# Kernel optimization log

Measured on AMD Instinct MI355X. Metric: run time of the kernel, lower is better.

The kernel has to match this reference:

```python
import jax, jax.numpy as jnp
import numpy as np

NUM_CLASSES = 1000
N, C = 8192, 256

def setup_inputs() -> dict:
    key = jax.random.key(0)
    k1, k2, k3 = jax.random.split(key, 3)
    p = jax.random.normal(k1, (N, C), dtype=jnp.float32)
    z = jax.random.normal(k2, (N, C), dtype=jnp.float32)
    t = jax.random.uniform(k3, (N, NUM_CLASSES), dtype=jnp.float32, minval=1e-4, maxval=1.0)
    targets = t / jnp.sum(t, axis=1, keepdims=True)  # valid soft-label distribution
    return {"p": p, "z": z, "targets": targets}

def reference(p, z, targets):
    z = jax.lax.stop_gradient(z)  # z.detach()
    # F.normalize(dim=1), eps=1e-12
    p = p / jnp.maximum(jnp.linalg.norm(p, axis=1, keepdims=True), 1e-12)
    zn = z / jnp.maximum(jnp.linalg.norm(z, axis=1, keepdims=True), 1e-12)
    dot_product = -jnp.matmul(p, zn.T)  # [N, N]
    # entropy of soft targets, NaN rows (any exact-zero entry) zeroed
    prod = targets * jnp.log(targets)
    entr = -jnp.sum(prod, axis=1)
    entr = jnp.where(jnp.isnan(entr), 0.0, entr)
    norm_entr = entr / jnp.log(jnp.float32(NUM_CLASSES))
    r = 1.0 - norm_entr
    mask1 = jnp.outer(r, r)  # [N, N]
    # cosine similarity Gram of targets (torch cosine_similarity eps=1e-8)
    tnorm = jnp.linalg.norm(targets, axis=1)
    denom = jnp.maximum(tnorm[:, None] * tnorm[None, :], 1e-8)
    mask2 = jnp.matmul(targets, targets.T) / denom  # [N, N]
    n = dot_product.shape[0]
    mask_anchor_out = 1.0 - jnp.eye(n, dtype=dot_product.dtype)
    mask_combined = mask1 * mask2 * mask_anchor_out
    sel = dot_product * mask_combined
    # mean over nonzero entries (jit-safe: sum / count of nonzeros)
    nz = (sel != 0.0)
    return jnp.sum(sel) / jnp.sum(nz).astype(sel.dtype)
```

## Files before the change

kernel.cpp:

```cpp
#include <hip/hip_runtime.h>
#include <math.h>

#define NROWS 8192
#define CDIM 256
#define KDIM 1000
#define KPAD 1024

#define BC 128
#define BK 64
#define BI 8

typedef __attribute__((ext_vector_type(8))) short bf16x8;
typedef __attribute__((ext_vector_type(4))) float f32x4;
typedef _Float16 f16;
typedef __attribute__((ext_vector_type(4))) _Float16 f16x4;

__device__ __forceinline__ unsigned short f2bf(float x) {
  unsigned int u = __float_as_uint(x);
  u += 0x7fffu + ((u >> 16) & 1u);
  return (unsigned short)(u >> 16);
}
__device__ __forceinline__ float bf2f(unsigned short h) {
  return __uint_as_float(((unsigned int)h) << 16);
}

__device__ __forceinline__ void gl16(const void* g, void* l) {
  __builtin_amdgcn_global_load_lds(
      (const __attribute__((address_space(1))) unsigned int*)g,
      (__attribute__((address_space(3))) unsigned int*)l, 16, 0, 0);
}

__global__ __launch_bounds__(256, 4) void prep_kernel(
    const float* __restrict__ p, const float* __restrict__ z,
    const float* __restrict__ t,
    unsigned short* __restrict__ gAhi, unsigned short* __restrict__ gAlo,
    unsigned short* __restrict__ gBhi, unsigned short* __restrict__ gBlo,
    unsigned short* __restrict__ gUhi, unsigned short* __restrict__ gUlo,
    float* __restrict__ diag) {
  __shared__ float tbuf[8 * 1028];
  __shared__ float st_s[8], uu_s[8], sa_s[8], sb_s[8];
  __shared__ double r_s[8];
  const int tid = threadIdx.x;
  const int w = tid >> 6, lane = tid & 63;
  const int stripe = blockIdx.x;
  const int istep = stripe >> 2;
  const int qtr = stripe & 3;
  const int i0 = stripe * 8;

#pragma unroll
  for (int rr = 0; rr < 2; ++rr) {
    const int row = 2 * w + rr;
    const float* trow = t + (size_t)(i0 + row) * KDIM;
    float stt = 0.f, ent = 0.f, zfl = 0.f;
#pragma unroll
    for (int c = 0; c < 4; ++c) {
      const int k4 = c * 64 + lane;
      float4 v = make_float4(0.f, 0.f, 0.f, 0.f);
      if (k4 < 250) {
        v = *(const float4*)(trow + k4 * 4);
        const float vv[4] = {v.x, v.y, v.z, v.w};
#pragma unroll
        for (int q = 0; q < 4; ++q) {
          stt += vv[q] * vv[q];
          if (vv[q] > 0.f) ent += vv[q] * logf(vv[q]);
          else zfl = 1.f;
        }
      }
      *(float4*)&tbuf[row * 1028 + k4 * 4] = v;
    }
#pragma unroll
    for (int off = 32; off; off >>= 1) {
      stt += __shfl_xor(stt, off);
      ent += __shfl_xor(ent, off);
      zfl += __shfl_xor(zfl, off);
    }
    if (lane == 0) {
      const float tnorm = sqrtf(stt);
      st_s[row] = 1.f / tnorm;
      uu_s[row] = stt / (tnorm * tnorm);
      const float entr = (zfl > 0.f) ? 0.f : (-ent);
      r_s[row] = 1.0 - (double)entr / log(1000.0);
    }
  }
  __syncthreads();

#pragma unroll
  for (int it = 0; it < 4; ++it) {
    const int item = it * 256 + tid;
    const int kt = item >> 7;
    const int kf = (item >> 4) & 7;
    const int cl = item & 15;
    const int kcl = kf * 16 + cl;
    unsigned int hi[4], lo[4];
#pragma unroll
    for (int q = 0; q < 4; ++q) {
      const int r0 = 2 * q, r1 = r0 + 1;
      const float v0 = tbuf[r0 * 1028 + kt * 128 + kcl] * st_s[r0];
      const float v1 = tbuf[r1 * 1028 + kt * 128 + kcl] * st_s[r1];
      const unsigned short h0 = f2bf(v0), h1 = f2bf(v1);
      hi[q] = (unsigned int)h0 | ((unsigned int)h1 << 16);
      const unsigned short e0 = f2bf(v0 - bf2f(h0));
      const unsigned short e1 = f2bf(v1 - bf2f(h1));
      lo[q] = (unsigned int)e0 | ((unsigned int)e1 << 16);
    }
    const size_t off = ((size_t)(kt * 256 + istep)) * 8192
                       + (size_t)kf * 1024 + (size_t)(qtr * 16 + cl) * 16;
    *(uint4*)((char*)gUhi + off) = make_uint4(hi[0], hi[1], hi[2], hi[3]);
    *(uint4*)((char*)gUlo + off) = make_uint4(lo[0], lo[1], lo[2], lo[3]);
  }
  __syncthreads();

  float* ptile = tbuf;
  float* ztile = tbuf + 8 * 260;
#pragma unroll
  for (int rr = 0; rr < 2; ++rr) {
    const int row = 2 * w + rr;
    const float* prow = p + (size_t)(i0 + row) * CDIM;
    const float* zrow = z + (size_t)(i0 + row) * CDIM;
    const float4 pv = *(const float4*)(prow + lane * 4);
    const float4 zv = *(const float4*)(zrow + lane * 4);
    *(float4*)&ptile[row * 260 + lane * 4] = pv;
    *(float4*)&ztile[row * 260 + lane * 4] = zv;
    float sp = pv.x * pv.x + pv.y * pv.y + pv.z * pv.z + pv.w * pv.w;
    float sz = zv.x * zv.x + zv.y * zv.y + zv.z * zv.z + zv.w * zv.w;
    float spz = pv.x * zv.x + pv.y * zv.y + pv.z * zv.z + pv.w * zv.w;
#pragma unroll
    for (int off = 32; off; off >>= 1) {
      sp += __shfl_xor(sp, off);
      sz += __shfl_xor(sz, off);
      spz += __shfl_xor(spz, off);
    }
    if (lane == 0) {
      const double r = r_s[row];
      const float pnorm = sqrtf(sp), znorm = sqrtf(sz);
      const float sav = (float)(r / fmax((double)pnorm, 1e-12));
      const float sbv = (float)(r / fmax((double)znorm, 1e-12));
      sa_s[row] = sav; sb_s[row] = sbv;
      diag[i0 + row] = spz * sav * sbv * uu_s[row];
    }
  }
  __syncthreads();

  {
    const int cfg = tid >> 4;
    const int cl = tid & 15;
    const int crd = cfg * 16 + cl;
#pragma unroll 1
    for (int which = 0; which < 2; ++which) {
      const float* tile = which ? ztile : ptile;
      const float* ss = which ? sb_s : sa_s;
      unsigned short* ghi = which ? gBhi : gAhi;
      unsigned short* glo = which ? gBlo : gAlo;
      unsigned int hi[4], lo[4];
#pragma unroll
      for (int q = 0; q < 4; ++q) {
        const int r0 = 2 * q, r1 = r0 + 1;
        const float v0 = tile[r0 * 260 + crd] * ss[r0];
        const float v1 = tile[r1 * 260 + crd] * ss[r1];
        const unsigned short h0 = f2bf(v0), h1 = f2bf(v1);
        hi[q] = (unsigned int)h0 | ((unsigned int)h1 << 16);
        const unsigned short e0 = f2bf(v0 - bf2f(h0));
        const unsigned short e1 = f2bf(v1 - bf2f(h1));
        lo[q] = (unsigned int)e0 | ((unsigned int)e1 << 16);
      }
      const size_t off = ((size_t)((cfg >> 3) * 256 + istep)) * 8192
                         + (size_t)(cfg & 7) * 1024 + (size_t)(qtr * 16 + cl) * 16;
      *(uint4*)((char*)ghi + off) = make_uint4(hi[0], hi[1], hi[2], hi[3]);
      *(uint4*)((char*)glo + off) = make_uint4(lo[0], lo[1], lo[2], lo[3]);
    }
  }
}

__global__ __launch_bounds__(256, 1) void mfma_gemm_kernel(
    const unsigned short* __restrict__ gAhi, const unsigned short* __restrict__ gAlo,
    const unsigned short* __restrict__ gBhi, const unsigned short* __restrict__ gBlo,
    const unsigned short* __restrict__ gUhi, const unsigned short* __restrict__ gUlo,
    f16* __restrict__ part1, f16* __restrict__ part2, int steps) {
  __shared__ unsigned short lds[3][6][4096];
  const int tid = threadIdx.x;
  const int lane = tid & 63;
  const int wid = tid >> 6;
  const int wr = wid >> 1, wc = wid & 1;
  const int ct = blockIdx.x, kt = blockIdx.y, zc = blockIdx.z;
  const int istep0 = zc * steps;

  f32x4 acc1[4][4], acc2[4][4];
#pragma unroll
  for (int c = 0; c < 4; ++c)
#pragma unroll
    for (int k = 0; k < 4; ++k) {
      acc1[c][k] = (f32x4){0.f, 0.f, 0.f, 0.f};
      acc2[c][k] = (f32x4){0.f, 0.f, 0.f, 0.f};
    }

  const char* sP[6] = {(const char*)gAhi, (const char*)gAlo,
                       (const char*)gBhi, (const char*)gBlo,
                       (const char*)gUhi, (const char*)gUlo};

  auto stage = [&](int buf, int s) {
    const size_t ab = ((size_t)(ct * 256 + istep0 + s)) * 8192 + (size_t)tid * 16;
    const size_t ub = ((size_t)(kt * 256 + istep0 + s)) * 8192 + (size_t)tid * 16;
#pragma unroll
    for (int pl = 0; pl < 4; ++pl) {
      gl16(sP[pl] + ab, &lds[buf][pl][tid * 8]);
      gl16(sP[pl] + ab + 4096, &lds[buf][pl][(tid + 256) * 8]);
    }
#pragma unroll
    for (int pl = 4; pl < 6; ++pl) {
      gl16(sP[pl] + ub, &lds[buf][pl][tid * 8]);
      gl16(sP[pl] + ub + 4096, &lds[buf][pl][(tid + 256) * 8]);
    }
  };

  stage(0, 0);
  if (steps > 1) stage(1, 1);
  for (int s = 0; s < steps; ++s) {
    const int cur = s % 3;
    if (s < steps - 1) {
      asm volatile("s_waitcnt vmcnt(12)" ::: "memory");
    } else {
      asm volatile("s_waitcnt vmcnt(0)" ::: "memory");
    }
    __builtin_amdgcn_s_barrier();
    asm volatile("" ::: "memory");
    if (s + 2 < steps) stage((s + 2) % 3, s + 2);

    bf16x8 ah[4], al[4], bh[4], bl[4];
#pragma unroll
    for (int c = 0; c < 4; ++c) {
      const int cf = wr * 4 + c;
      ah[c] = *(const bf16x8*)&lds[cur][0][(cf * 64 + lane) * 8];
      al[c] = *(const bf16x8*)&lds[cur][1][(cf * 64 + lane) * 8];
      bh[c] = *(const bf16x8*)&lds[cur][2][(cf * 64 + lane) * 8];
      bl[c] = *(const bf16x8*)&lds[cur][3][(cf * 64 + lane) * 8];
    }
    __builtin_amdgcn_s_setprio(1);
#pragma unroll
    for (int kh = 0; kh < 2; ++kh) {
      bf16x8 uh[2], ul[2];
#pragma unroll
      for (int k2 = 0; k2 < 2; ++k2) {
        const int kf = wc * 4 + kh * 2 + k2;
        uh[k2] = *(const bf16x8*)&lds[cur][4][(kf * 64 + lane) * 8];
        ul[k2] = *(const bf16x8*)&lds[cur][5][(kf * 64 + lane) * 8];
      }
#pragma unroll
      for (int k2 = 0; k2 < 2; ++k2) {
        const int k = kh * 2 + k2;
#pragma unroll
        for (int c = 0; c < 4; ++c) {
          acc1[c][k] = __builtin_amdgcn_mfma_f32_16x16x32_bf16(ah[c], uh[k2], acc1[c][k], 0, 0, 0);
          acc1[c][k] = __builtin_amdgcn_mfma_f32_16x16x32_bf16(al[c], uh[k2], acc1[c][k], 0, 0, 0);
          acc1[c][k] = __builtin_amdgcn_mfma_f32_16x16x32_bf16(ah[c], ul[k2], acc1[c][k], 0, 0, 0);
          acc2[c][k] = __builtin_amdgcn_mfma_f32_16x16x32_bf16(bh[c], uh[k2], acc2[c][k], 0, 0, 0);
          acc2[c][k] = __builtin_amdgcn_mfma_f32_16x16x32_bf16(bl[c], uh[k2], acc2[c][k], 0, 0, 0);
          acc2[c][k] = __builtin_amdgcn_mfma_f32_16x16x32_bf16(bh[c], ul[k2], acc2[c][k], 0, 0, 0);
        }
      }
    }
    __builtin_amdgcn_s_setprio(0);
  }

  f16* o1 = part1 + (size_t)zc * (CDIM * KPAD);
  f16* o2 = part2 + (size_t)zc * (CDIM * KPAD);
#pragma unroll
  for (int c = 0; c < 4; ++c)
#pragma unroll
    for (int k = 0; k < 4; ++k)
#pragma unroll
      for (int j = 0; j < 4; ++j) {
        const int cg = ct * 128 + (wr * 4 + c) * 16 + (lane >> 4) * 4 + j;
        const int kg = kt * 128 + (wc * 4 + k) * 16 + (lane & 15);
        o1[(size_t)cg * KPAD + kg] = (f16)acc1[c][k][j];
        o2[(size_t)cg * KPAD + kg] = (f16)acc2[c][k][j];
      }
}

__global__ __launch_bounds__(256) void reduce_h_kernel(
    const f16* __restrict__ part1, const f16* __restrict__ part2,
    double* __restrict__ bsum, int split) {
  const int tid = threadIdx.x;
  const size_t base = ((size_t)blockIdx.x * 256 + tid) * 4;
  double m1[4] = {0, 0, 0, 0}, m2[4] = {0, 0, 0, 0};
#pragma unroll 4
  for (int zz = 0; zz < split; ++zz) {
    const f16x4 a = *(const f16x4*)(part1 + (size_t)zz * (CDIM * KPAD) + base);
    const f16x4 b = *(const f16x4*)(part2 + (size_t)zz * (CDIM * KPAD) + base);
#pragma unroll
    for (int e = 0; e < 4; ++e) {
      m1[e] += (double)(float)a[e];
      m2[e] += (double)(float)b[e];
    }
  }
  double s = 0.0;
#pragma unroll
  for (int e = 0; e < 4; ++e) s += m1[e] * m2[e];
  __shared__ double red[256];
  red[tid] = s;
  __syncthreads();
  for (int off = 128; off; off >>= 1) {
    if (tid < off) red[tid] += red[tid + off];
    __syncthreads();
  }
  if (tid == 0) bsum[blockIdx.x] = red[0];
}

__global__ __launch_bounds__(256) void rowstats_kernel(
    const float* __restrict__ p, const float* __restrict__ z,
    const float* __restrict__ t,
    float* __restrict__ sa, float* __restrict__ sb,
    float* __restrict__ st, float* __restrict__ diag) {
  const int i = blockIdx.x;
  const int tid = threadIdx.x;
  const float pv = p[(size_t)i * CDIM + tid];
  const float zv = z[(size_t)i * CDIM + tid];
  float sp = pv * pv, sz = zv * zv, spz = pv * zv;
  float stt = 0.f, ent = 0.f, zfl = 0.f;
  const float* trow = t + (size_t)i * KDIM;
  for (int k = tid; k < KDIM; k += 256) {
    const float tv = trow[k];
    stt += tv * tv;
    if (tv > 0.f) ent += tv * logf(tv);
    else zfl = 1.f;
  }
#pragma unroll
  for (int off = 32; off; off >>= 1) {
    sp  += __shfl_down(sp, off);
    sz  += __shfl_down(sz, off);
    spz += __shfl_down(spz, off);
    stt += __shfl_down(stt, off);
    ent += __shfl_down(ent, off);
    zfl += __shfl_down(zfl, off);
  }
  __shared__ float wred[4][6];
  const int wid = tid >> 6, lane = tid & 63;
  if (lane == 0) {
    wred[wid][0] = sp;  wred[wid][1] = sz;  wred[wid][2] = spz;
    wred[wid][3] = stt; wred[wid][4] = ent; wred[wid][5] = zfl;
  }
  __syncthreads();
  if (tid == 0) {
    sp  = wred[0][0] + wred[1][0] + wred[2][0] + wred[3][0];
    sz  = wred[0][1] + wred[1][1] + wred[2][1] + wred[3][1];
    spz = wred[0][2] + wred[1][2] + wred[2][2] + wred[3][2];
    stt = wred[0][3] + wred[1][3] + wred[2][3] + wred[3][3];
    ent = wred[0][4] + wred[1][4] + wred[2][4] + wred[3][4];
    zfl = wred[0][5] + wred[1][5] + wred[2][5] + wred[3][5];
    const float pnorm = sqrtf(sp);
    const float znorm = sqrtf(sz);
    const float tnorm = sqrtf(stt);
    const float entr = (zfl > 0.f) ? 0.f : (-ent);
    const double r = 1.0 - (double)entr / log(1000.0);
    const float sav = (float)(r / fmax((double)pnorm, 1e-12));
    const float sbv = (float)(r / fmax((double)znorm, 1e-12));
    const float stv = 1.f / tnorm;
    const float uu = stt / (tnorm * tnorm);
    sa[i] = sav; sb[i] = sbv; st[i] = stv;
    diag[i] = spz * sav * sbv * uu;
  }
}

__global__ __launch_bounds__(256) void fp32_gemm_kernel(
    const float* __restrict__ p, const float* __restrict__ z,
    const float* __restrict__ t,
    const float* __restrict__ sa, const float* __restrict__ sb,
    const float* __restrict__ st,
    float* __restrict__ part1, float* __restrict__ part2, int ichunk) {
  __shared__ float As[BI][BC];
  __shared__ float Bs[BI][BC];
  __shared__ float Us[BI][BK];
  const int tid = threadIdx.x;
  const int c0 = blockIdx.x * BC;
  const int k0 = blockIdx.y * BK;
  const int i0 = blockIdx.z * ichunk;
  float acc1[8][4] = {{0.f}};
  float acc2[8][4] = {{0.f}};
  const int tc = tid & 15;
  const int tk = tid >> 4;
  const int lrow = tid >> 5;
  const int lcolA = (tid & 31) * 4;
  const int lcolU = (tid & 31) * 2;
  for (int ib = 0; ib < ichunk; ib += BI) {
    const int i = i0 + ib + lrow;
    const float sav = sa[i], sbv = sb[i], stv = st[i];
    const float4 pv = *(const float4*)(p + (size_t)i * CDIM + c0 + lcolA);
    const float4 zv = *(const float4*)(z + (size_t)i * CDIM + c0 + lcolA);
    const int kk = k0 + lcolU;
    const float u0 = (kk     < KDIM) ? t[(size_t)i * KDIM + kk]     * stv : 0.f;
    const float u1 = (kk + 1 < KDIM) ? t[(size_t)i * KDIM + kk + 1] * stv : 0.f;
    __syncthreads();
    *(float4*)&As[lrow][lcolA] = make_float4(pv.x * sav, pv.y * sav, pv.z * sav, pv.w * sav);
    *(float4*)&Bs[lrow][lcolA] = make_float4(zv.x * sbv, zv.y * sbv, zv.z * sbv, zv.w * sbv);
    Us[lrow][lcolU] = u0;
    Us[lrow][lcolU + 1] = u1;
    __syncthreads();
#pragma unroll
    for (int ii = 0; ii < BI; ++ii) {
      const float4 a0 = *(const float4*)&As[ii][tc * 8];
      const float4 a1 = *(const float4*)&As[ii][tc * 8 + 4];
      const float4 b0 = *(const float4*)&Bs[ii][tc * 8];
      const float4 b1 = *(const float4*)&Bs[ii][tc * 8 + 4];
      const float4 u  = *(const float4*)&Us[ii][tk * 4];
      const float a[8] = {a0.x, a0.y, a0.z, a0.w, a1.x, a1.y, a1.z, a1.w};
      const float b[8] = {b0.x, b0.y, b0.z, b0.w, b1.x, b1.y, b1.z, b1.w};
      const float uv[4] = {u.x, u.y, u.z, u.w};
#pragma unroll
      for (int m = 0; m < 8; ++m)
#pragma unroll
        for (int n = 0; n < 4; ++n) {
          acc1[m][n] = fmaf(a[m], uv[n], acc1[m][n]);
          acc2[m][n] = fmaf(b[m], uv[n], acc2[m][n]);
        }
    }
  }
  float* o1 = part1 + (size_t)blockIdx.z * (CDIM * KPAD);
  float* o2 = part2 + (size_t)blockIdx.z * (CDIM * KPAD);
#pragma unroll
  for (int m = 0; m < 8; ++m) {
    const int c = c0 + tc * 8 + m;
    const int k = k0 + tk * 4;
    *(float4*)&o1[(size_t)c * KPAD + k] = *(const float4*)acc1[m];
    *(float4*)&o2[(size_t)c * KPAD + k] = *(const float4*)acc2[m];
  }
}

__global__ __launch_bounds__(256) void reduce_kernel(
    const float* __restrict__ part1, const float* __restrict__ part2,
    double* __restrict__ bsum, int split) {
  const int tid = threadIdx.x;
  double s = 0.0;
  for (int r = 0; r < 4; ++r) {
    const size_t idx = (size_t)blockIdx.x * 1024 + (size_t)r * 256 + tid;
    double m1 = 0.0, m2 = 0.0;
    for (int zz = 0; zz < split; ++zz) {
      m1 += (double)part1[(size_t)zz * (CDIM * KPAD) + idx];
      m2 += (double)part2[(size_t)zz * (CDIM * KPAD) + idx];
    }
    s += m1 * m2;
  }
  __shared__ double red[256];
  red[tid] = s;
  __syncthreads();
  for (int off = 128; off; off >>= 1) {
    if (tid < off) red[tid] += red[tid + off];
    __syncthreads();
  }
  if (tid == 0) bsum[blockIdx.x] = red[0];
}

__global__ __launch_bounds__(256) void final_kernel(
    const double* __restrict__ bsum, const float* __restrict__ diag,
    float* __restrict__ out, int nb) {
  const int tid = threadIdx.x;
  double s = 0.0;
  for (int i = tid; i < nb; i += 256) s += bsum[i];
  double d = 0.0;
  for (int i = tid; i < NROWS; i += 256) d += (double)diag[i];
  __shared__ double red[256];
  red[tid] = s;
  __syncthreads();
  for (int off = 128; off; off >>= 1) {
    if (tid < off) red[tid] += red[tid + off];
    __syncthreads();
  }
  double s_all = red[0];
  __syncthreads();
  red[tid] = d;
  __syncthreads();
  for (int off = 128; off; off >>= 1) {
    if (tid < off) red[tid] += red[tid + off];
    __syncthreads();
  }
  if (tid == 0) {
    const double s_diag = red[0];
    const double sel_sum = -(s_all - s_diag);
    const double cnt = (double)NROWS * (double)NROWS - (double)NROWS;
    out[0] = (float)(sel_sum / cnt);
  }
}

extern "C" void kernel_launch(void* const* d_in, const int* in_sizes, int n_in,
                              void* d_out, int out_size, void* d_ws, size_t ws_size,
                              hipStream_t stream) {
  const float* p = (const float*)d_in[0];
  const float* z = (const float*)d_in[1];
  const float* t = (const float*)d_in[2];
  float* out = (float*)d_out;
  char* ws = (char*)d_ws;

  float* sa = (float*)ws;
  float* sb = sa + NROWS;
  float* st = sb + NROWS;
  float* diag = st + NROWS;
  const size_t statsB = (size_t)4 * NROWS * sizeof(float);

  const size_t planeA = (size_t)2 * 256 * 8 * 1024;
  const size_t planeU = (size_t)8 * 256 * 8 * 1024;
  const size_t chunkH = (size_t)CDIM * KPAD * 2;
  const size_t chunkF = (size_t)CDIM * KPAD * 4;

  int split = 16;
  while (split > 4 &&
         statsB + 4 * planeA + 2 * planeU + (size_t)split * 2 * chunkH + 8192 > ws_size)
    split >>= 1;
  const bool use_mfma =
      statsB + 4 * planeA + 2 * planeU + (size_t)split * 2 * chunkH + 8192 <= ws_size;

  if (use_mfma) {
    char* base = ws + statsB;
    unsigned short* gAhi = (unsigned short*)(base);
    unsigned short* gAlo = (unsigned short*)(base + planeA);
    unsigned short* gBhi = (unsigned short*)(base + 2 * planeA);
    unsigned short* gBlo = (unsigned short*)(base + 3 * planeA);
    unsigned short* gUhi = (unsigned short*)(base + 4 * planeA);
    unsigned short* gUlo = (unsigned short*)(base + 4 * planeA + planeU);
    f16* part1 = (f16*)(base + 4 * planeA + 2 * planeU);
    f16* part2 = part1 + (size_t)split * (CDIM * KPAD);
    double* bsum = (double*)(part2 + (size_t)split * (CDIM * KPAD));
    const int steps = (NROWS / split) / 32;

    hipLaunchKernelGGL(prep_kernel, dim3(1024), dim3(256), 0, stream,
                       p, z, t, gAhi, gAlo, gBhi, gBlo, gUhi, gUlo, diag);
    hipLaunchKernelGGL(mfma_gemm_kernel, dim3(2, 8, split), dim3(256), 0, stream,
                       gAhi, gAlo, gBhi, gBlo, gUhi, gUlo, part1, part2, steps);
    hipLaunchKernelGGL(reduce_h_kernel, dim3(256), dim3(256), 0, stream,
                       part1, part2, bsum, split);
    hipLaunchKernelGGL(final_kernel, dim3(1), dim3(256), 0, stream,
                       bsum, diag, out, 256);
  } else {
    int osplit = 16;
    while (osplit > 1 &&
           statsB + (size_t)osplit * chunkF * 2 + 8192 > ws_size)
      osplit >>= 1;
    float* part1 = (float*)(ws + statsB);
    float* part2 = part1 + (size_t)osplit * (CDIM * KPAD);
    double* bsum = (double*)(part2 + (size_t)osplit * (CDIM * KPAD));
    hipLaunchKernelGGL(rowstats_kernel, dim3(NROWS), dim3(256), 0, stream,
                       p, z, t, sa, sb, st, diag);
    hipLaunchKernelGGL(fp32_gemm_kernel, dim3(CDIM / BC, KPAD / BK, osplit),
                       dim3(256), 0, stream,
                       p, z, t, sa, sb, st, part1, part2, NROWS / osplit);
    hipLaunchKernelGGL(reduce_kernel, dim3(256), dim3(256), 0, stream,
                       part1, part2, bsum, osplit);
    hipLaunchKernelGGL(final_kernel, dim3(1), dim3(256), 0, stream,
                       bsum, diag, out, 256);
  }
}
```

Baseline: 65.62 us.

## Widen MFMA GEMM blocks to 512 threads with double-buffered LDS and doubled split

```diff
diff --git a/kernel.cpp b/kernel.cpp
--- a/kernel.cpp
+++ b/kernel.cpp
@@ -87,7 +87,7 @@
 #pragma unroll
   for (int it = 0; it < 4; ++it) {
     const int item = it * 256 + tid;
-    const int kt = item >> 7;
+    const int kt8 = item >> 7;
     const int kf = (item >> 4) & 7;
     const int cl = item & 15;
     const int kcl = kf * 16 + cl;
@@ -95,15 +95,15 @@
 #pragma unroll
     for (int q = 0; q < 4; ++q) {
       const int r0 = 2 * q, r1 = r0 + 1;
-      const float v0 = tbuf[r0 * 1028 + kt * 128 + kcl] * st_s[r0];
-      const float v1 = tbuf[r1 * 1028 + kt * 128 + kcl] * st_s[r1];
+      const float v0 = tbuf[r0 * 1028 + kt8 * 128 + kcl] * st_s[r0];
+      const float v1 = tbuf[r1 * 1028 + kt8 * 128 + kcl] * st_s[r1];
       const unsigned short h0 = f2bf(v0), h1 = f2bf(v1);
       hi[q] = (unsigned int)h0 | ((unsigned int)h1 << 16);
       const unsigned short e0 = f2bf(v0 - bf2f(h0));
       const unsigned short e1 = f2bf(v1 - bf2f(h1));
       lo[q] = (unsigned int)e0 | ((unsigned int)e1 << 16);
     }
-    const size_t off = ((size_t)(kt * 256 + istep)) * 8192
+    const size_t off = ((size_t)(kt8 * 256 + istep)) * 8192
                        + (size_t)kf * 1024 + (size_t)(qtr * 16 + cl) * 16;
     *(uint4*)((char*)gUhi + off) = make_uint4(hi[0], hi[1], hi[2], hi[3]);
     *(uint4*)((char*)gUlo + off) = make_uint4(lo[0], lo[1], lo[2], lo[3]);
@@ -171,12 +171,12 @@
   }
 }
 
-__global__ __launch_bounds__(256, 1) void mfma_gemm_kernel(
+__global__ __launch_bounds__(512, 1) void mfma_gemm_kernel(
     const unsigned short* __restrict__ gAhi, const unsigned short* __restrict__ gAlo,
     const unsigned short* __restrict__ gBhi, const unsigned short* __restrict__ gBlo,
     const unsigned short* __restrict__ gUhi, const unsigned short* __restrict__ gUlo,
     f16* __restrict__ part1, f16* __restrict__ part2, int steps) {
-  __shared__ unsigned short lds[3][6][4096];
+  __shared__ unsigned short lds[2][32768];
   const int tid = threadIdx.x;
   const int lane = tid & 63;
   const int wid = tid >> 6;
@@ -184,71 +184,67 @@
   const int ct = blockIdx.x, kt = blockIdx.y, zc = blockIdx.z;
   const int istep0 = zc * steps;
 
-  f32x4 acc1[4][4], acc2[4][4];
-#pragma unroll
-  for (int c = 0; c < 4; ++c)
-#pragma unroll
-    for (int k = 0; k < 4; ++k) {
+  f32x4 acc1[2][8], acc2[2][8];
+#pragma unroll
+  for (int c = 0; c < 2; ++c)
+#pragma unroll
+    for (int k = 0; k < 8; ++k) {
       acc1[c][k] = (f32x4){0.f, 0.f, 0.f, 0.f};
       acc2[c][k] = (f32x4){0.f, 0.f, 0.f, 0.f};
     }
 
-  const char* sP[6] = {(const char*)gAhi, (const char*)gAlo,
-                       (const char*)gBhi, (const char*)gBlo,
-                       (const char*)gUhi, (const char*)gUlo};
+  const char* sA[4] = {(const char*)gAhi, (const char*)gAlo,
+                       (const char*)gBhi, (const char*)gBlo};
 
   auto stage = [&](int buf, int s) {
     const size_t ab = ((size_t)(ct * 256 + istep0 + s)) * 8192 + (size_t)tid * 16;
-    const size_t ub = ((size_t)(kt * 256 + istep0 + s)) * 8192 + (size_t)tid * 16;
-#pragma unroll
-    for (int pl = 0; pl < 4; ++pl) {
-      gl16(sP[pl] + ab, &lds[buf][pl][tid * 8]);
-      gl16(sP[pl] + ab + 4096, &lds[buf][pl][(tid + 256) * 8]);
-    }
-#pragma unroll
-    for (int pl = 4; pl < 6; ++pl) {
-      gl16(sP[pl] + ub, &lds[buf][pl][tid * 8]);
-      gl16(sP[pl] + ub + 4096, &lds[buf][pl][(tid + 256) * 8]);
-    }
+    const size_t ub0 = ((size_t)((2 * kt) * 256 + istep0 + s)) * 8192 + (size_t)tid * 16;
+    const size_t ub1 = ((size_t)((2 * kt + 1) * 256 + istep0 + s)) * 8192 + (size_t)tid * 16;
+#pragma unroll
+    for (int pl = 0; pl < 4; ++pl)
+      gl16(sA[pl] + ab, &lds[buf][pl * 4096 + tid * 8]);
+    gl16((const char*)gUhi + ub0, &lds[buf][16384 + tid * 8]);
+    gl16((const char*)gUhi + ub1, &lds[buf][16384 + 4096 + tid * 8]);
+    gl16((const char*)gUlo + ub0, &lds[buf][24576 + tid * 8]);
+    gl16((const char*)gUlo + ub1, &lds[buf][24576 + 4096 + tid * 8]);
   };
 
   stage(0, 0);
-  if (steps > 1) stage(1, 1);
   for (int s = 0; s < steps; ++s) {
-    const int cur = s % 3;
-    if (s < steps - 1) {
-      asm volatile("s_waitcnt vmcnt(12)" ::: "memory");
+    const int cur = s & 1;
+    if (s + 1 < steps) {
+      stage(cur ^ 1, s + 1);
+      asm volatile("s_waitcnt vmcnt(8)" ::: "memory");
     } else {
       asm volatile("s_waitcnt vmcnt(0)" ::: "memory");
     }
     __builtin_amdgcn_s_barrier();
     asm volatile("" ::: "memory");
-    if (s + 2 < steps) stage((s + 2) % 3, s + 2);
-
-    bf16x8 ah[4], al[4], bh[4], bl[4];
-#pragma unroll
-    for (int c = 0; c < 4; ++c) {
-      const int cf = wr * 4 + c;
-      ah[c] = *(const bf16x8*)&lds[cur][0][(cf * 64 + lane) * 8];
-      al[c] = *(const bf16x8*)&lds[cur][1][(cf * 64 + lane) * 8];
-      bh[c] = *(const bf16x8*)&lds[cur][2][(cf * 64 + lane) * 8];
-      bl[c] = *(const bf16x8*)&lds[cur][3][(cf * 64 + lane) * 8];
+
+    bf16x8 ah[2], al[2], bh[2], bl[2];
+#pragma unroll
+    for (int c = 0; c < 2; ++c) {
+      const int cf = wr * 2 + c;
+      ah[c] = *(const bf16x8*)&lds[cur][0 * 4096 + (cf * 64 + lane) * 8];
+      al[c] = *(const bf16x8*)&lds[cur][1 * 4096 + (cf * 64 + lane) * 8];
+      bh[c] = *(const bf16x8*)&lds[cur][2 * 4096 + (cf * 64 + lane) * 8];
+      bl[c] = *(const bf16x8*)&lds[cur][3 * 4096 + (cf * 64 + lane) * 8];
     }
     __builtin_amdgcn_s_setprio(1);
 #pragma unroll
-    for (int kh = 0; kh < 2; ++kh) {
+    for (int kh = 0; kh < 4; ++kh) {
       bf16x8 uh[2], ul[2];
 #pragma unroll
       for (int k2 = 0; k2 < 2; ++k2) {
-        const int kf = wc * 4 + kh * 2 + k2;
-        uh[k2] = *(const bf16x8*)&lds[cur][4][(kf * 64 + lane) * 8];
-        ul[k2] = *(const bf16x8*)&lds[cur][5][(kf * 64 + lane) * 8];
+        const int kfg = wc * 8 + kh * 2 + k2;
+        uh[k2] = *(const bf16x8*)&lds[cur][16384 + (kfg * 64 + lane) * 8];
+        ul[k2] = *(const bf16x8*)&lds[cur][24576 + (kfg * 64 + lane) * 8];
       }
 #pragma unroll
       for (int k2 = 0; k2 < 2; ++k2) {
         const int k = kh * 2 + k2;
 #pragma unroll
-        for (int c = 0; c < 4; ++c) {
+        for (int c = 0; c < 2; ++c) {
           acc1[c][k] = __builtin_amdgcn_mfma_f32_16x16x32_bf16(ah[c], uh[k2], acc1[c][k], 0, 0, 0);
           acc1[c][k] = __builtin_amdgcn_mfma_f32_16x16x32_bf16(al[c], uh[k2], acc1[c][k], 0, 0, 0);
           acc1[c][k] = __builtin_amdgcn_mfma_f32_16x16x32_bf16(ah[c], ul[k2], acc1[c][k], 0, 0, 0);
@@ -259,18 +255,19 @@
       }
     }
     __builtin_amdgcn_s_setprio(0);
+    __builtin_amdgcn_s_barrier();
   }
 
   f16* o1 = part1 + (size_t)zc * (CDIM * KPAD);
   f16* o2 = part2 + (size_t)zc * (CDIM * KPAD);
 #pragma unroll
-  for (int c = 0; c < 4; ++c)
-#pragma unroll
-    for (int k = 0; k < 4; ++k)
+  for (int c = 0; c < 2; ++c)
+#pragma unroll
+    for (int k = 0; k < 8; ++k)
 #pragma unroll
       for (int j = 0; j < 4; ++j) {
-        const int cg = ct * 128 + (wr * 4 + c) * 16 + (lane >> 4) * 4 + j;
-        const int kg = kt * 128 + (wc * 4 + k) * 16 + (lane & 15);
+        const int cg = ct * 128 + (wr * 2 + c) * 16 + (lane >> 4) * 4 + j;
+        const int kg = kt * 256 + (wc * 8 + k) * 16 + (lane & 15);
         o1[(size_t)cg * KPAD + kg] = (f16)acc1[c][k][j];
         o2[(size_t)cg * KPAD + kg] = (f16)acc2[c][k][j];
       }
@@ -499,7 +496,7 @@
   const size_t chunkH = (size_t)CDIM * KPAD * 2;
   const size_t chunkF = (size_t)CDIM * KPAD * 4;
 
-  int split = 16;
+  int split = 32;
   while (split > 4 &&
          statsB + 4 * planeA + 2 * planeU + (size_t)split * 2 * chunkH + 8192 > ws_size)
     split >>= 1;
@@ -521,7 +518,7 @@
 
     hipLaunchKernelGGL(prep_kernel, dim3(1024), dim3(256), 0, stream,
                        p, z, t, gAhi, gAlo, gBhi, gBlo, gUhi, gUlo, diag);
-    hipLaunchKernelGGL(mfma_gemm_kernel, dim3(2, 8, split), dim3(256), 0, stream,
+    hipLaunchKernelGGL(mfma_gemm_kernel, dim3(2, 4, split), dim3(512), 0, stream,
                        gAhi, gAlo, gBhi, gBlo, gUhi, gUlo, part1, part2, steps);
     hipLaunchKernelGGL(reduce_h_kernel, dim3(256), dim3(256), 0, stream,
                        part1, part2, bsum, split);
```

Result: slower. 70.43 us (+7.3%).
